# Performance work log

Hardware: AMD Instinct MI355X
Metric: run time of the kernel (lower is better)

## Reference

```python
import jax, jax.numpy as jnp
import numpy as np

N = 100_000   # nodes
E = 1_600_000 # edges (avg degree 16)
F_IN = 64
H = 64


def gcn_conv(x, row, col, dinv, W, b, n):
    # PyG GCNConv: out = D^{-1/2} (A+I) D^{-1/2} (x @ W) + b
    # row/col already include self-loops; dinv = deg^{-1/2} precomputed per layer caller
    norm = dinv[row] * dinv[col]            # [E+N]
    h = x @ W                               # [N, H] small GEMM
    msg = h[row] * norm[:, None]            # [E+N, H] gather + scale
    out = jax.ops.segment_sum(msg, col, num_segments=n)  # scatter-add
    return out + b


def setup_inputs() -> dict:
    key = jax.random.key(0)
    ks = jax.random.split(key, 8)
    x = jax.random.normal(ks[0], (N, F_IN), jnp.float32)
    edge_index = jax.random.randint(ks[1], (2, E), 0, N, dtype=jnp.int32)
    s = 1.0 / np.sqrt(F_IN)
    W1 = jax.random.normal(ks[2], (F_IN, H), jnp.float32) * s
    b1 = jnp.zeros((H,), jnp.float32)
    W2 = jax.random.normal(ks[3], (H, H), jnp.float32) * s
    b2 = jnp.zeros((H,), jnp.float32)
    W3 = jax.random.normal(ks[4], (H, H), jnp.float32) * s
    b3 = jnp.zeros((H,), jnp.float32)
    return {"x": x, "edge_index": edge_index, "W1": W1, "b1": b1,
            "W2": W2, "b2": b2, "W3": W3, "b3": b3}


def reference(x, edge_index, W1, b1, W2, b2, W3, b3):
    n = x.shape[0]
    loop = jnp.arange(n, dtype=edge_index.dtype)
    row = jnp.concatenate([edge_index[0], loop])  # sources (+ self loops)
    col = jnp.concatenate([edge_index[1], loop])  # targets (+ self loops)
    deg = jax.ops.segment_sum(jnp.ones_like(col, x.dtype), col, num_segments=n)
    dinv = jnp.where(deg > 0, jax.lax.rsqrt(deg), 0.0)

    h = gcn_conv(x, row, col, dinv, W1, b1, n)
    h = jax.nn.elu(h)
    # dropout: eval mode -> identity
    h = gcn_conv(h, row, col, dinv, W2, b2, n)
    h = jax.nn.elu(h)
    h = gcn_conv(h, row, col, dinv, W3, b3, n)
    return h
```

## Files before the change

kernel.cpp:

```cpp
#include <hip/hip_runtime.h>
#include <hip/hip_bf16.h>
#include <math.h>


#define FDIM 64
#define BKT 128
#define MAXNB 1024
#define BCAP 4080

typedef float f32x2 __attribute__((ext_vector_type(2)));


__global__ __launch_bounds__(1024) void partB_kernel(const int* __restrict__ erow,
                                                     const int* __restrict__ ecol,
                                                     int* __restrict__ cursor,
                                                     int* __restrict__ extra,
                                                     unsigned* __restrict__ part,
                                                     int e, int nb, int epb) {
    __shared__ int lh[MAXNB];
    __shared__ int lbase[MAXNB];
    const int t = threadIdx.x;
    for (int i = t; i < nb; i += 1024) lh[i] = 0;
    __syncthreads();
    int s = blockIdx.x * epb;
    int en = s + epb; if (en > e) en = e;
    for (int i = s + t; i < en; i += 1024) atomicAdd(&lh[ecol[i] >> 7], 1);
    __syncthreads();
    for (int i = t; i < nb; i += 1024)
        lbase[i] = lh[i] ? atomicAdd(&cursor[i], lh[i]) : 0;
    __syncthreads();
    for (int i = t; i < nb; i += 1024) lh[i] = 0;
    __syncthreads();
    for (int i = s + t; i < en; i += 1024) {
        int c = ecol[i];
        int b = c >> 7;
        int pos = lbase[b] + atomicAdd(&lh[b], 1);
        if (pos < BCAP) part[(size_t)b * BCAP + pos] = ((unsigned)erow[i] << 7) | (unsigned)(c & 127);
        else atomicAdd(&extra[c], 1);
    }
}

__global__ __launch_bounds__(256) void adjw_kernel(const unsigned* __restrict__ part,
                                                   const int* __restrict__ cursor,
                                                   const int* __restrict__ extra,
                                                   int* __restrict__ cnt,
                                                   int* __restrict__ adjF,
                                                   int n, int cap) {
    const int b = blockIdx.x;
    const int v0 = b << 7;
    __shared__ int lc[BKT];
    const int t = threadIdx.x;
    if (t < BKT) lc[t] = 0;
    __syncthreads();
    int tot = cursor[b];
    int s1 = (tot < BCAP) ? tot : BCAP;
    const unsigned* __restrict__ pb = part + (size_t)b * BCAP;
    for (int e = t; e < s1; e += 256) {
        unsigned pk = pb[e];
        int c = pk & 127;
        int slot = atomicAdd(&lc[c], 1);
        if (slot < cap) adjF[(size_t)(v0 + c) * cap + slot] = (int)(pk >> 7);
    }
    __syncthreads();
    int nn = n - v0; if (nn > BKT) nn = BKT;
    if (t < nn) {
        int ex = extra[v0 + t];
        int d = lc[t] + ex;
        cnt[v0 + t] = (ex > 0) ? -d : d;
    }
}


__global__ __launch_bounds__(256) void gemm_kernel(const float* __restrict__ X,
                                                   const float* __restrict__ W,
                                                   const int* __restrict__ cnt,
                                                   __hip_bfloat16* __restrict__ Hout, int n) {
    __shared__ float XT[64][68];
    __shared__ float Ws[64][68];
    const int t = threadIdx.x;
    const int row0 = blockIdx.x * 64;
    #pragma unroll
    for (int i = t; i < 4096; i += 256) Ws[i >> 6][i & 63] = W[i];
    #pragma unroll
    for (int i = t; i < 4096; i += 256) {
        int r = i >> 6, c = i & 63;
        int gr = row0 + r;
        XT[c][r] = (gr < n) ? X[(size_t)gr * FDIM + c] : 0.0f;
    }
    __syncthreads();

    const int tc = t & 15;
    const int tr = t >> 4;
    float acc[4][4];
    #pragma unroll
    for (int i = 0; i < 4; i++)
        #pragma unroll
        for (int j = 0; j < 4; j++) acc[i][j] = 0.0f;

    #pragma unroll 8
    for (int k = 0; k < 64; k++) {
        float4 a = *(const float4*)&XT[k][4 * tr];
        float4 b = *(const float4*)&Ws[k][4 * tc];
        acc[0][0] += a.x * b.x; acc[0][1] += a.x * b.y; acc[0][2] += a.x * b.z; acc[0][3] += a.x * b.w;
        acc[1][0] += a.y * b.x; acc[1][1] += a.y * b.y; acc[1][2] += a.y * b.z; acc[1][3] += a.y * b.w;
        acc[2][0] += a.z * b.x; acc[2][1] += a.z * b.y; acc[2][2] += a.z * b.z; acc[2][3] += a.z * b.w;
        acc[3][0] += a.w * b.x; acc[3][1] += a.w * b.y; acc[3][2] += a.w * b.z; acc[3][3] += a.w * b.w;
    }

    #pragma unroll
    for (int i = 0; i < 4; i++) {
        int gr = row0 + 4 * tr + i;
        if (gr < n) {
            float dv = rsqrtf(fabsf((float)cnt[gr]) + 1.0f);
            union { ushort4 u; __hip_bfloat16 h[4]; } pk;
            pk.h[0] = __float2bfloat16(acc[i][0] * dv);
            pk.h[1] = __float2bfloat16(acc[i][1] * dv);
            pk.h[2] = __float2bfloat16(acc[i][2] * dv);
            pk.h[3] = __float2bfloat16(acc[i][3] * dv);
            *(ushort4*)&Hout[(size_t)gr * FDIM + 4 * tc] = pk.u;
        }
    }
}

__device__ inline f32x2 bf2f(unsigned u) {
    f32x2 r;
    r.x = __uint_as_float(u << 16);
    r.y = __uint_as_float(u & 0xffff0000u);
    return r;
}

__device__ inline void unpack_add(uint4 w, f32x2* a) {
    a[0] += bf2f(w.x);
    a[1] += bf2f(w.y);
    a[2] += bf2f(w.z);
    a[3] += bf2f(w.w);
}

__global__ __launch_bounds__(256) void agg_kernel(const __hip_bfloat16* __restrict__ hs,
                                                  const int* __restrict__ adjF,
                                                  const int* __restrict__ cnt,
                                                  const float* __restrict__ bias,
                                                  float* __restrict__ out,
                                                  int n, int cap, int do_elu,
                                                  const int* __restrict__ erow,
                                                  const int* __restrict__ ecol, int etot) {
    const int v = blockIdx.x * 4 + (threadIdx.x >> 6);
    const int lane = threadIdx.x & 63;
    if (v >= n) return;
    const int sl = lane & 7;
    const int es = lane >> 3;
    const int deg_raw = cnt[v];
    const int deg = (deg_raw < 0) ? -deg_raw : deg_raw;
    const float dv = rsqrtf((float)deg + 1.0f);
    const uint4* __restrict__ hs4 = (const uint4*)hs;

    f32x2 a[4];
    #pragma unroll
    for (int j = 0; j < 4; j++) a[j] = (f32x2)(0.0f);

    if (es == 0) {
        uint4 w = hs4[(size_t)v * 8 + sl];
        unpack_add(w, a);
    }

    if (deg_raw >= 0 && deg_raw <= cap) {
        const int* __restrict__ av = adjF + (size_t)v * cap;
        int m = deg;
        int uvec = 0;
        if (lane < m) uvec = av[lane];
        int g = 0;
        for (; g + 16 <= m; g += 16) {
            int u0 = __shfl(uvec, g + es, 64);
            int u1 = __shfl(uvec, g + 8 + es, 64);
            uint4 w0 = hs4[(size_t)u0 * 8 + sl];
            uint4 w1 = hs4[(size_t)u1 * 8 + sl];
            unpack_add(w0, a);
            unpack_add(w1, a);
        }
        for (; g < m; g += 8) {
            int idx = g + es;
            int u = __shfl(uvec, (idx < m) ? idx : 0, 64);
            if (idx < m) {
                uint4 w = hs4[(size_t)u * 8 + sl];
                unpack_add(w, a);
            }
        }
    } else {
        for (int base = 0; base < etot; base += 64) {
            int m = etot - base; if (m > 64) m = 64;
            int c = -1, r = 0;
            if (lane < m) { c = ecol[base + lane]; r = erow[base + lane]; }
            unsigned long long mask = __ballot(c == v);
            while (mask) {
                int j = __ffsll((long long)mask) - 1;
                mask &= mask - 1;
                int u = __shfl(r, j, 64);
                if (es == 0) {
                    uint4 w = hs4[(size_t)u * 8 + sl];
                    unpack_add(w, a);
                }
            }
        }
    }

    #pragma unroll
    for (int off = 8; off < 64; off <<= 1) {
        #pragma unroll
        for (int j = 0; j < 4; j++) {
            f32x2 o;
            o.x = __shfl_xor(a[j].x, off, 64);
            o.y = __shfl_xor(a[j].y, off, 64);
            a[j] += o;
        }
    }

    if (es == 0) {
        const f32x2* b2 = (const f32x2*)&bias[8 * sl];
        float r[8];
        #pragma unroll
        for (int j = 0; j < 4; j++) {
            f32x2 tv = a[j] * dv + b2[j];
            r[2 * j] = tv.x;
            r[2 * j + 1] = tv.y;
        }
        if (do_elu) {
            #pragma unroll
            for (int j = 0; j < 8; j++)
                r[j] = (r[j] > 0.0f) ? r[j] : (__expf(r[j]) - 1.0f);
        }
        float4* op = (float4*)&out[(size_t)v * FDIM + 8 * sl];
        op[0] = make_float4(r[0], r[1], r[2], r[3]);
        op[1] = make_float4(r[4], r[5], r[6], r[7]);
    }
}


extern "C" void kernel_launch(void* const* d_in, const int* in_sizes, int n_in,
                              void* d_out, int out_size, void* d_ws, size_t ws_size,
                              hipStream_t stream) {
    const float* x   = (const float*)d_in[0];
    const int*   ei  = (const int*)d_in[1];
    const float* W1  = (const float*)d_in[2];
    const float* b1  = (const float*)d_in[3];
    const float* W2  = (const float*)d_in[4];
    const float* b2  = (const float*)d_in[5];
    const float* W3  = (const float*)d_in[6];
    const float* b3  = (const float*)d_in[7];

    const int N = in_sizes[0] / FDIM;
    const int E = in_sizes[1] / 2;
    const int* erow = ei;
    const int* ecol = ei + E;

    const int NB = (N + BKT - 1) / BKT;

    char* p = (char*)d_ws;
    __hip_bfloat16* hsb = (__hip_bfloat16*)p;  p += (size_t)N * FDIM * sizeof(__hip_bfloat16);
    int*   cnt  = (int*)p;   p += (size_t)N * sizeof(int);
    int* cursor = (int*)p;   p += (size_t)(NB + 1) * sizeof(int);
    int* extra  = (int*)p;   p += (size_t)N * sizeof(int);
    int*   adjF = (int*)p;

    unsigned* part = (unsigned*)hsb;

    size_t used = (size_t)(p - (char*)d_ws);
    int cap = 64;
    while (cap > 32 && used + (size_t)N * cap * sizeof(int) > ws_size) cap -= 16;

    float* outb = (float*)d_out;

    const int TB = 256;
    const int PBLK = 256;
    const int epb = (E + PBLK - 1) / PBLK;
    const int nblkG = (N + 63) / 64;
    const int nblkA = (N + 3) / 4;

    hipMemsetAsync(cursor, 0, (size_t)(NB + 1 + N) * sizeof(int), stream);
    partB_kernel<<<PBLK, 1024, 0, stream>>>(erow, ecol, cursor, extra, part, E, NB, epb);
    adjw_kernel<<<NB, TB, 0, stream>>>(part, cursor, extra, cnt, adjF, N, cap);

    gemm_kernel<<<nblkG, TB, 0, stream>>>(x, W1, cnt, hsb, N);
    agg_kernel<<<nblkA, TB, 0, stream>>>(hsb, adjF, cnt, b1, outb, N, cap, 1, erow, ecol, E);
    gemm_kernel<<<nblkG, TB, 0, stream>>>(outb, W2, cnt, hsb, N);
    agg_kernel<<<nblkA, TB, 0, stream>>>(hsb, adjF, cnt, b2, outb, N, cap, 1, erow, ecol, E);
    gemm_kernel<<<nblkG, TB, 0, stream>>>(outb, W3, cnt, hsb, N);
    agg_kernel<<<nblkA, TB, 0, stream>>>(hsb, adjF, cnt, b3, outb, N, cap, 0, erow, ecol, E);
}
```

Baseline: 327.8 us.

## Use 32-lane half-wave per node in aggregation with 8-way unrolled gathers

The aggregation kernel now gives each destination node 32 lanes. Each lane owns two bf16 features and loads 4 bytes per neighbor, replacing the old scheme of 8 edge-slots by 8 lanes with 16-byte loads followed by a cross-lane shuffle reduction. Neighbor indices are broadcast within the half-wave and up to 8 gathers are issued back to back, which removes the final xor-shuffle reduction and doubles nodes per block. The trade-off is narrower per-lane loads, which may need more memory instructions per row. The slow fallback path is restructured to work per half-wave.

```diff
diff --git a/kernel.cpp b/kernel.cpp
--- a/kernel.cpp
+++ b/kernel.cpp
@@ -129,13 +129,6 @@
     return r;
 }
 
-__device__ inline void unpack_add(uint4 w, f32x2* a) {
-    a[0] += bf2f(w.x);
-    a[1] += bf2f(w.y);
-    a[2] += bf2f(w.z);
-    a[3] += bf2f(w.w);
-}
-
 __global__ __launch_bounds__(256) void agg_kernel(const __hip_bfloat16* __restrict__ hs,
                                                   const int* __restrict__ adjF,
                                                   const int* __restrict__ cnt,
@@ -144,93 +137,90 @@
                                                   int n, int cap, int do_elu,
                                                   const int* __restrict__ erow,
                                                   const int* __restrict__ ecol, int etot) {
-    const int v = blockIdx.x * 4 + (threadIdx.x >> 6);
-    const int lane = threadIdx.x & 63;
-    if (v >= n) return;
-    const int sl = lane & 7;
-    const int es = lane >> 3;
-    const int deg_raw = cnt[v];
-    const int deg = (deg_raw < 0) ? -deg_raw : deg_raw;
-    const float dv = rsqrtf((float)deg + 1.0f);
-    const uint4* __restrict__ hs4 = (const uint4*)hs;
-
-    f32x2 a[4];
-    #pragma unroll
-    for (int j = 0; j < 4; j++) a[j] = (f32x2)(0.0f);
-
-    if (es == 0) {
-        uint4 w = hs4[(size_t)v * 8 + sl];
-        unpack_add(w, a);
-    }
-
-    if (deg_raw >= 0 && deg_raw <= cap) {
+    const int tid = threadIdx.x;
+    const int v = blockIdx.x * 8 + (tid >> 5);
+    const int lane32 = tid & 31;
+    const int half = (tid >> 5) & 1;
+    const bool alive = v < n;
+    const unsigned* __restrict__ hsu = (const unsigned*)hs;
+
+    int deg_raw = alive ? cnt[v] : 0;
+    int deg = (deg_raw < 0) ? -deg_raw : deg_raw;
+    bool slow = alive && (deg_raw < 0 || deg > cap);
+
+    f32x2 a = (f32x2)(0.0f);
+    if (alive) a = bf2f(hsu[(size_t)v * 32 + lane32]);
+
+    if (alive && !slow) {
         const int* __restrict__ av = adjF + (size_t)v * cap;
-        int m = deg;
-        int uvec = 0;
-        if (lane < m) uvec = av[lane];
-        int g = 0;
-        for (; g + 16 <= m; g += 16) {
-            int u0 = __shfl(uvec, g + es, 64);
-            int u1 = __shfl(uvec, g + 8 + es, 64);
-            uint4 w0 = hs4[(size_t)u0 * 8 + sl];
-            uint4 w1 = hs4[(size_t)u1 * 8 + sl];
-            unpack_add(w0, a);
-            unpack_add(w1, a);
-        }
-        for (; g < m; g += 8) {
-            int idx = g + es;
-            int u = __shfl(uvec, (idx < m) ? idx : 0, 64);
-            if (idx < m) {
-                uint4 w = hs4[(size_t)u * 8 + sl];
-                unpack_add(w, a);
-            }
-        }
-    } else {
-        for (int base = 0; base < etot; base += 64) {
-            int m = etot - base; if (m > 64) m = 64;
+        for (int base = 0; base < deg; base += 32) {
+            int mc = deg - base; if (mc > 32) mc = 32;
+            int uvec = 0;
+            if (lane32 < mc) uvec = av[base + lane32];
+            int g = 0;
+            for (; g + 8 <= mc; g += 8) {
+                int u0 = __shfl(uvec, g + 0, 32);
+                int u1 = __shfl(uvec, g + 1, 32);
+                int u2 = __shfl(uvec, g + 2, 32);
+                int u3 = __shfl(uvec, g + 3, 32);
+                int u4 = __shfl(uvec, g + 4, 32);
+                int u5 = __shfl(uvec, g + 5, 32);
+                int u6 = __shfl(uvec, g + 6, 32);
+                int u7 = __shfl(uvec, g + 7, 32);
+                unsigned w0 = hsu[(size_t)u0 * 32 + lane32];
+                unsigned w1 = hsu[(size_t)u1 * 32 + lane32];
+                unsigned w2 = hsu[(size_t)u2 * 32 + lane32];
+                unsigned w3 = hsu[(size_t)u3 * 32 + lane32];
+                unsigned w4 = hsu[(size_t)u4 * 32 + lane32];
+                unsigned w5 = hsu[(size_t)u5 * 32 + lane32];
+                unsigned w6 = hsu[(size_t)u6 * 32 + lane32];
+                unsigned w7 = hsu[(size_t)u7 * 32 + lane32];
+                a += bf2f(w0); a += bf2f(w1); a += bf2f(w2); a += bf2f(w3);
+                a += bf2f(w4); a += bf2f(w5); a += bf2f(w6); a += bf2f(w7);
+            }
+            for (; g + 4 <= mc; g += 4) {
+                int u0 = __shfl(uvec, g + 0, 32);
+                int u1 = __shfl(uvec, g + 1, 32);
+                int u2 = __shfl(uvec, g + 2, 32);
+                int u3 = __shfl(uvec, g + 3, 32);
+                unsigned w0 = hsu[(size_t)u0 * 32 + lane32];
+                unsigned w1 = hsu[(size_t)u1 * 32 + lane32];
+                unsigned w2 = hsu[(size_t)u2 * 32 + lane32];
+                unsigned w3 = hsu[(size_t)u3 * 32 + lane32];
+                a += bf2f(w0); a += bf2f(w1); a += bf2f(w2); a += bf2f(w3);
+            }
+            for (; g < mc; g++) {
+                int u = __shfl(uvec, g, 32);
+                a += bf2f(hsu[(size_t)u * 32 + lane32]);
+            }
+        }
+    }
+    if (__any(slow)) {
+        for (int base = 0; base < etot; base += 32) {
+            int m = etot - base; if (m > 32) m = 32;
             int c = -1, r = 0;
-            if (lane < m) { c = ecol[base + lane]; r = erow[base + lane]; }
-            unsigned long long mask = __ballot(c == v);
-            while (mask) {
-                int j = __ffsll((long long)mask) - 1;
-                mask &= mask - 1;
-                int u = __shfl(r, j, 64);
-                if (es == 0) {
-                    uint4 w = hs4[(size_t)u * 8 + sl];
-                    unpack_add(w, a);
-                }
-            }
-        }
-    }
-
-    #pragma unroll
-    for (int off = 8; off < 64; off <<= 1) {
-        #pragma unroll
-        for (int j = 0; j < 4; j++) {
-            f32x2 o;
-            o.x = __shfl_xor(a[j].x, off, 64);
-            o.y = __shfl_xor(a[j].y, off, 64);
-            a[j] += o;
-        }
-    }
-
-    if (es == 0) {
-        const f32x2* b2 = (const f32x2*)&bias[8 * sl];
-        float r[8];
-        #pragma unroll
-        for (int j = 0; j < 4; j++) {
-            f32x2 tv = a[j] * dv + b2[j];
-            r[2 * j] = tv.x;
-            r[2 * j + 1] = tv.y;
-        }
+            if (lane32 < m) { c = ecol[base + lane32]; r = erow[base + lane32]; }
+            unsigned long long b = __ballot(slow && (c == v));
+            unsigned bh = (unsigned)(b >> (half * 32));
+            while (bh) {
+                int j = __ffs(bh) - 1;
+                bh &= bh - 1;
+                int u = __shfl(r, j, 32);
+                if (slow) a += bf2f(hsu[(size_t)u * 32 + lane32]);
+            }
+        }
+    }
+
+    if (alive) {
+        float dv = rsqrtf((float)deg + 1.0f);
+        f32x2 bv = ((const f32x2*)bias)[lane32];
+        f32x2 rr = a * dv + bv;
+        float rx = rr.x, ry = rr.y;
         if (do_elu) {
-            #pragma unroll
-            for (int j = 0; j < 8; j++)
-                r[j] = (r[j] > 0.0f) ? r[j] : (__expf(r[j]) - 1.0f);
-        }
-        float4* op = (float4*)&out[(size_t)v * FDIM + 8 * sl];
-        op[0] = make_float4(r[0], r[1], r[2], r[3]);
-        op[1] = make_float4(r[4], r[5], r[6], r[7]);
+            rx = (rx > 0.0f) ? rx : (__expf(rx) - 1.0f);
+            ry = (ry > 0.0f) ? ry : (__expf(ry) - 1.0f);
+        }
+        ((float2*)out)[(size_t)v * 32 + lane32] = make_float2(rx, ry);
     }
 }
 
@@ -273,7 +263,7 @@
     const int PBLK = 256;
     const int epb = (E + PBLK - 1) / PBLK;
     const int nblkG = (N + 63) / 64;
-    const int nblkA = (N + 3) / 4;
+    const int nblkA = (N + 7) / 8;
 
     hipMemsetAsync(cursor, 0, (size_t)(NB + 1 + N) * sizeof(int), stream);
     partB_kernel<<<PBLK, 1024, 0, stream>>>(erow, ecol, cursor, extra, part, E, NB, epb);
```

Result: faster. 320.4 us (-2.2%).
